# Kernel tuning notes

Hardware: AMD Instinct MI355X
Metric: run time of the kernel (lower is better)

The kernel has to match this reference:

```python
import jax, jax.numpy as jnp
import numpy as np

N, E = 50000, 800000
IN_FEATS, H, L = 16, 64, 3


def _glorot(key, shape):
    fan_in = shape[-1]
    return jax.random.normal(key, shape, dtype=jnp.float32) / np.sqrt(fan_in)


def setup_inputs() -> dict:
    key = jax.random.key(0)
    ks = jax.random.split(key, 12)
    return {
        "features": jax.random.normal(ks[0], (N, IN_FEATS), dtype=jnp.float32),
        "src": jax.random.randint(ks[1], (E,), 0, N, dtype=jnp.int32),
        "dst": jax.random.randint(ks[2], (E,), 0, N, dtype=jnp.int32),
        # input_module: Linear(in_feats, hidden)
        "W_in": _glorot(ks[3], (IN_FEATS, H)),
        "b_in": jnp.zeros((H,), jnp.float32),
        # edge_module: Linear(2*hidden, 1), shared across layers
        "W_edge": _glorot(ks[4], (2 * H, 1)),
        "b_edge": jnp.zeros((1,), jnp.float32),
        # per-layer GRUCell params (torch layout: [3H, H] for W_ih/W_hh)
        "Wih": _glorot(ks[5], (L, 3 * H, H)),
        "Whh": _glorot(ks[6], (L, 3 * H, H)),
        "bih": jnp.zeros((L, 3 * H), jnp.float32),
        "bhh": jnp.zeros((L, 3 * H), jnp.float32),
        # edge_predictor: Linear(2*hidden, 1)
        "W_pred": _glorot(ks[7], (2 * H, 1)),
        "b_pred": jnp.zeros((1,), jnp.float32),
    }


def _gru_cell(x, h, W_ih, W_hh, b_ih, b_hh):
    # torch.nn.GRUCell math
    gi = x @ W_ih.T + b_ih  # [N, 3H]
    gh = h @ W_hh.T + b_hh  # [N, 3H]
    i_r, i_z, i_n = jnp.split(gi, 3, axis=1)
    h_r, h_z, h_n = jnp.split(gh, 3, axis=1)
    r = jax.nn.sigmoid(i_r + h_r)
    z = jax.nn.sigmoid(i_z + h_z)
    n = jnp.tanh(i_n + r * h_n)
    return (1.0 - z) * n + z * h


def reference(features, src, dst, W_in, b_in, W_edge, b_edge, Wih, Whh, bih, bhh, W_pred, b_pred):
    n_nodes = features.shape[0]
    h = features @ W_in + b_in  # [N, H]
    num_layers = Wih.shape[0]
    for l in range(num_layers):
        h_u = h[src]  # [E, H] gather src
        h_v = h[dst]  # [E, H] gather dst
        # shared edge module: sigmoid(Linear(cat[h_u, h_v]))
        w = jax.nn.sigmoid(jnp.concatenate([h_u, h_v], axis=1) @ W_edge + b_edge)  # [E, 1]
        m = h_u * w  # messages [E, H]
        h_new = jax.ops.segment_sum(m, dst, num_segments=n_nodes)  # scatter-sum to dst
        h = _gru_cell(h_new, h, Wih[l], Whh[l], bih[l], bhh[l])
    edges_h = jnp.concatenate([h[src], h[dst]], axis=1)  # [E, 2H]
    return (edges_h @ W_pred + b_pred).squeeze()  # [E]
```

## Files before the change

### kernel.cpp

```cpp
#include <hip/hip_runtime.h>
#include <hip/hip_bf16.h>

#define H 64
#define H3 192
#define ITEMS 16

typedef __attribute__((ext_vector_type(8))) short short8;
typedef __attribute__((ext_vector_type(4))) float f32x4;

__device__ __forceinline__ float sigmoidf_(float x) {
    return 1.0f / (1.0f + __expf(-x));
}
__device__ __forceinline__ float tanhf_(float x) {
    float e = __expf(2.0f * x);
    return 1.0f - 2.0f / (e + 1.0f);
}
__device__ __forceinline__ unsigned short f2bf(float f) {
    unsigned u = __builtin_bit_cast(unsigned, f);
    u += 0x7FFFu + ((u >> 16) & 1u);
    return (unsigned short)(u >> 16);
}
__device__ __forceinline__ float bf2f(unsigned short s) {
    return __builtin_bit_cast(float, (unsigned)s << 16);
}

__global__ __launch_bounds__(256) void setup_kernel(
    const float* __restrict__ feat, const float* __restrict__ Win,
    const float* __restrict__ bin, const float* __restrict__ Wg,
    unsigned short* __restrict__ h_bf,
    float* __restrict__ a_gate, float* __restrict__ b_gate,
    const float* __restrict__ Wih, const float* __restrict__ Whh,
    unsigned short* __restrict__ w_bf,
    const int* __restrict__ dst, int* __restrict__ bhist,
    int N, int E, int per, int nbA, int nbB, int nb_c)
{
    int bid = blockIdx.x;
    int t = threadIdx.x;
    if (bid < nbA) {
        __shared__ float sWin[16 * H];
        __shared__ float sbin[H];
        __shared__ float sWg[2 * H];
        for (int i = t; i < 16 * H; i += 256) sWin[i] = Win[i];
        if (t < H) sbin[t] = bin[t];
        if (t < 2 * H) sWg[t] = Wg[t];
        __syncthreads();

        int n = bid * 256 + t;
        if (n >= N) return;

        float f[16];
        const float4* fr = (const float4*)(feat + (size_t)n * 16);
#pragma unroll
        for (int i = 0; i < 4; i++) {
            float4 v = fr[i];
            f[4 * i + 0] = v.x; f[4 * i + 1] = v.y;
            f[4 * i + 2] = v.z; f[4 * i + 3] = v.w;
        }
        float a = 0.f, b = 0.f;
        unsigned short* brow = h_bf + (size_t)n * H;
        for (int j = 0; j < H; j++) {
            float hj = sbin[j];
#pragma unroll
            for (int k = 0; k < 16; k++) hj += f[k] * sWin[k * H + j];
            brow[j] = f2bf(hj);
            a += hj * sWg[j];
            b += hj * sWg[H + j];
        }
        a_gate[n] = a;
        b_gate[n] = b;
    } else if (bid < nbA + nbB) {
        int i = (bid - nbA) * 256 + t;
        if (i < per) w_bf[i] = f2bf(Wih[i]);
        else if (i < 2 * per) w_bf[i] = f2bf(Whh[i - per]);
    } else {
        __shared__ int lh[256];
        lh[t] = 0;
        __syncthreads();
        int base = (bid - nbA - nbB) * (256 * ITEMS);
#pragma unroll
        for (int k = 0; k < ITEMS; k++) {
            int i = base + k * 256 + t;
            if (i < E) atomicAdd(&lh[dst[i] >> 8], 1);
        }
        __syncthreads();
        bhist[t * nb_c + (bid - nbA - nbB)] = lh[t];
    }
}

__global__ __launch_bounds__(256) void scan_fused(
    const int* __restrict__ bhist, int* __restrict__ S, int M, int E)
{
    int t = threadIdx.x;
    int b = blockIdx.x;
    int pre = b * 256;
    if (pre > M) pre = M;
    int v = 0;
    for (int k = t; k < pre; k += 256) v += bhist[k];
#pragma unroll
    for (int off = 32; off >= 1; off >>= 1) v += __shfl_xor(v, off);
    __shared__ int ws[4];
    if ((t & 63) == 0) ws[t >> 6] = v;
    __syncthreads();
    int carry = ws[0] + ws[1] + ws[2] + ws[3];

    int i = b * 256 + t;
    int x = (i < M) ? bhist[i] : 0;
    int lane = t & 63, w = t >> 6;
    int s = x;
#pragma unroll
    for (int off = 1; off < 64; off <<= 1) {
        int u = __shfl_up(s, off);
        if (lane >= off) s += u;
    }
    __shared__ int wsum[4];
    if (lane == 63) wsum[w] = s;
    __syncthreads();
    int add = 0;
    for (int k = 0; k < w; k++) add += wsum[k];
    if (i < M) S[i] = carry + s + add - x;
    else if (i == M) S[M] = E;
}

__global__ __launch_bounds__(256) void bucket_scatter_kernel(
    const int* __restrict__ src, const int* __restrict__ dst,
    const int* __restrict__ S, unsigned* __restrict__ pk, int E, int nb_c)
{
    __shared__ int lbase[256];
    __shared__ int lrun[256];
    int t = threadIdx.x;
    lbase[t] = S[t * nb_c + blockIdx.x];
    lrun[t] = 0;
    __syncthreads();
    int base = blockIdx.x * (256 * ITEMS);
#pragma unroll
    for (int k = 0; k < ITEMS; k++) {
        int i = base + k * 256 + t;
        if (i < E) {
            int d = dst[i];
            int b = d >> 8;
            int r = atomicAdd(&lrun[b], 1);
            pk[lbase[b] + r] = ((unsigned)(d & 255) << 16) | (unsigned)src[i];
        }
    }
}

__global__ __launch_bounds__(256) void bucket_finalize_kernel(
    const unsigned* __restrict__ pk, const int* __restrict__ S,
    int* __restrict__ offsets, unsigned short* __restrict__ csr16,
    int N, int E, int nb_c, int NB)
{
    __shared__ int lh[256];
    __shared__ int loff[256];
    __shared__ int lrun[256];
    int t = threadIdx.x;
    int b = blockIdx.x;
    int beg = S[b * nb_c];
    int endb = (b + 1 < NB) ? S[(b + 1) * nb_c] : E;
    lh[t] = 0; lrun[t] = 0;
    __syncthreads();
    for (int i = beg + t; i < endb; i += 256) atomicAdd(&lh[pk[i] >> 16], 1);
    __syncthreads();
    int v = lh[t];
    loff[t] = v;
    __syncthreads();
    for (int off = 1; off < 256; off <<= 1) {
        int u = (t >= off) ? loff[t - off] : 0;
        __syncthreads();
        loff[t] += u;
        __syncthreads();
    }
    int excl = loff[t] - v;
    int node = b * 256 + t;
    if (node < N) offsets[node] = beg + excl;
    if (b == NB - 1 && t == 0) offsets[N] = E;
    loff[t] = excl;
    __syncthreads();
    for (int i = beg + t; i < endb; i += 256) {
        unsigned w = pk[i];
        int d = (int)(w >> 16);
        int r = atomicAdd(&lrun[d], 1);
        csr16[beg + loff[d] + r] = (unsigned short)(w & 0xFFFFu);
    }
}

__global__ __launch_bounds__(256) void aggregate_kernel(
    const unsigned short* __restrict__ h_bf, const float* __restrict__ a_gate,
    const float* __restrict__ b_gate, const int* __restrict__ offsets,
    const unsigned short* __restrict__ csr16, const float* __restrict__ b_edge,
    unsigned short* __restrict__ hnew_bf, int N)
{
    int wid = threadIdx.x >> 6;
    int lane = threadIdx.x & 63;
    int sub = lane >> 3;
    int cg  = lane & 7;
    int v = blockIdx.x * 4 + wid;
    if (v >= N) return;

    int beg = offsets[v];
    int end = offsets[v + 1];
    float bv = b_gate[v] + b_edge[0];
    float acc0[8] = {0.f, 0.f, 0.f, 0.f, 0.f, 0.f, 0.f, 0.f};
    float acc1[8] = {0.f, 0.f, 0.f, 0.f, 0.f, 0.f, 0.f, 0.f};

    for (int cs = beg; cs < end; cs += 64) {
        int m = end - cs; if (m > 64) m = 64;
        int u = 0; float w = 0.f;
        if (lane < m) {
            u = (int)csr16[cs + lane];
            w = sigmoidf_(a_gate[u] + bv);
        }
        for (int j = 0; j < m; j += 16) {
            int e0 = j + sub, e1 = j + 8 + sub;
            int u0 = __shfl(u, e0 & 63);
            float w0 = __shfl(w, e0 & 63);
            int u1 = __shfl(u, e1 & 63);
            float w1 = __shfl(w, e1 & 63);
            if (e0 >= m) w0 = 0.f;
            if (e1 >= m) w1 = 0.f;
            short8 hv0 = *(const short8*)(h_bf + (size_t)u0 * H + cg * 8);
            short8 hv1 = *(const short8*)(h_bf + (size_t)u1 * H + cg * 8);
#pragma unroll
            for (int k = 0; k < 8; k++)
                acc0[k] += w0 * bf2f((unsigned short)hv0[k]);
#pragma unroll
            for (int k = 0; k < 8; k++)
                acc1[k] += w1 * bf2f((unsigned short)hv1[k]);
        }
    }
#pragma unroll
    for (int k = 0; k < 8; k++) acc0[k] += acc1[k];
#pragma unroll
    for (int mm = 8; mm < 64; mm <<= 1) {
#pragma unroll
        for (int k = 0; k < 8; k++)
            acc0[k] += __shfl_xor(acc0[k], mm);
    }
    if (sub == 0) {
        short8 o;
#pragma unroll
        for (int k = 0; k < 8; k++) o[k] = (short)f2bf(acc0[k]);
        *(short8*)(hnew_bf + (size_t)v * H + cg * 8) = o;
    }
}

__global__ __launch_bounds__(256) void gru_mfma_kernel(
    const unsigned short* __restrict__ x_bf,
    unsigned short* __restrict__ h_bf,
    const unsigned short* __restrict__ wih_bf,
    const unsigned short* __restrict__ whh_bf,
    const float* __restrict__ bih, const float* __restrict__ bhh,
    const float* __restrict__ Wg,
    float* __restrict__ a_gate, float* __restrict__ b_gate, int N)
{
    int lane = threadIdx.x & 63;
    int wv = threadIdx.x >> 6;
    int c = lane & 15;
    int g = lane >> 4;
    int nbase = blockIdx.x * 64 + wv * 16;
    if (nbase >= N) return;

    int nrow = nbase + c;
    int nclamp = nrow < N ? nrow : (N - 1);

    short8 ax[2], ah[2];
#pragma unroll
    for (int ch = 0; ch < 2; ch++) {
        ax[ch] = *(const short8*)(x_bf + (size_t)nclamp * H + ch * 32 + g * 8);
        ah[ch] = *(const short8*)(h_bf + (size_t)nclamp * H + ch * 32 + g * 8);
    }

    f32x4 gi[12], gh[12];
#pragma unroll
    for (int jb = 0; jb < 12; jb++) {
        gi[jb] = (f32x4){0.f, 0.f, 0.f, 0.f};
        gh[jb] = (f32x4){0.f, 0.f, 0.f, 0.f};
    }

#pragma unroll
    for (int jb = 0; jb < 12; jb++) {
        const unsigned short* wi = wih_bf + (size_t)(jb * 16 + c) * H + g * 8;
        const unsigned short* wh = whh_bf + (size_t)(jb * 16 + c) * H + g * 8;
        short8 wi0 = *(const short8*)(wi);
        short8 wi1 = *(const short8*)(wi + 32);
        short8 wh0 = *(const short8*)(wh);
        short8 wh1 = *(const short8*)(wh + 32);
        gi[jb] = __builtin_amdgcn_mfma_f32_16x16x32_bf16(ax[0], wi0, gi[jb], 0, 0, 0);
        gi[jb] = __builtin_amdgcn_mfma_f32_16x16x32_bf16(ax[1], wi1, gi[jb], 0, 0, 0);
        gh[jb] = __builtin_amdgcn_mfma_f32_16x16x32_bf16(ah[0], wh0, gh[jb], 0, 0, 0);
        gh[jb] = __builtin_amdgcn_mfma_f32_16x16x32_bf16(ah[1], wh1, gh[jb], 0, 0, 0);
    }

    float pa[4] = {0.f, 0.f, 0.f, 0.f};
    float pb[4] = {0.f, 0.f, 0.f, 0.f};
#pragma unroll
    for (int jb = 0; jb < 4; jb++) {
        int j = jb * 16 + c;
        float br = bih[j] + bhh[j];
        float bz = bih[H + j] + bhh[H + j];
        float bin_ = bih[2 * H + j];
        float bhn_ = bhh[2 * H + j];
        float wga = Wg[j], wgb = Wg[H + j];
#pragma unroll
        for (int q = 0; q < 4; q++) {
            int node = nbase + g * 4 + q;
            float r = sigmoidf_(gi[jb][q] + gh[jb][q] + br);
            float z = sigmoidf_(gi[jb + 4][q] + gh[jb + 4][q] + bz);
            float nn = tanhf_(gi[jb + 8][q] + bin_ + r * (gh[jb + 8][q] + bhn_));
            size_t idx = (size_t)node * H + j;
            float hp = bf2f(h_bf[idx]);
            float ho = (1.0f - z) * nn + z * hp;
            h_bf[idx] = f2bf(ho);
            pa[q] += ho * wga;
            pb[q] += ho * wgb;
        }
    }
#pragma unroll
    for (int m = 1; m < 16; m <<= 1) {
#pragma unroll
        for (int q = 0; q < 4; q++) {
            pa[q] += __shfl_xor(pa[q], m);
            pb[q] += __shfl_xor(pb[q], m);
        }
    }
    if (c == 0) {
#pragma unroll
        for (int q = 0; q < 4; q++) {
            int node = nbase + g * 4 + q;
            a_gate[node] = pa[q];
            b_gate[node] = pb[q];
        }
    }
}

__global__ __launch_bounds__(256) void predict_kernel(
    const int* __restrict__ src, const int* __restrict__ dst,
    const float* __restrict__ pa, const float* __restrict__ pb,
    const float* __restrict__ b_pred, float* __restrict__ out, int E)
{
    int e4 = (blockIdx.x * 256 + threadIdx.x) * 4;
    float bp = b_pred[0];
    if (e4 + 3 < E) {
        int4 s = *(const int4*)(src + e4);
        int4 d = *(const int4*)(dst + e4);
        float4 o;
        o.x = pa[s.x] + pb[d.x] + bp;
        o.y = pa[s.y] + pb[d.y] + bp;
        o.z = pa[s.z] + pb[d.z] + bp;
        o.w = pa[s.w] + pb[d.w] + bp;
        *(float4*)(out + e4) = o;
    } else {
        for (int e = e4; e < E; e++)
            out[e] = pa[src[e]] + pb[dst[e]] + bp;
    }
}

extern "C" void kernel_launch(void* const* d_in, const int* in_sizes, int n_in,
                              void* d_out, int out_size, void* d_ws, size_t ws_size,
                              hipStream_t stream) {
    const float* features = (const float*)d_in[0];
    const int*   src      = (const int*)d_in[1];
    const int*   dst      = (const int*)d_in[2];
    const float* W_in     = (const float*)d_in[3];
    const float* b_in     = (const float*)d_in[4];
    const float* W_edge   = (const float*)d_in[5];
    const float* b_edge   = (const float*)d_in[6];
    const float* Wih      = (const float*)d_in[7];
    const float* Whh      = (const float*)d_in[8];
    const float* bih      = (const float*)d_in[9];
    const float* bhh      = (const float*)d_in[10];
    const float* W_pred   = (const float*)d_in[11];
    const float* b_pred   = (const float*)d_in[12];
    float* out = (float*)d_out;

    int N = in_sizes[0] / 16;
    int E = in_sizes[1];
    int L = in_sizes[7] / (H3 * H);
    int per = L * H3 * H;

    int nb_nodes = (N + 255) / 256;
    int nb_agg   = (N + 3) / 4;
    int nb_gru   = (N + 63) / 64;
    int nb_conv  = (2 * per + 255) / 256;
    int nb_pred  = (E + 1023) / 1024;

    int nb_c = (E + 256 * ITEMS - 1) / (256 * ITEMS);
    int NB   = (N + 255) / 256;
    int M    = 256 * nb_c;
    int nb_scan = (M + 1 + 255) / 256;

    unsigned short* h_bf = (unsigned short*)d_ws;
    unsigned short* hnew_bf = h_bf + (size_t)N * H;
    unsigned short* w_bf = hnew_bf + (size_t)N * H;
    float* a_gate = (float*)(w_bf + 2 * per);
    float* b_gate = a_gate + N;
    int* offsets  = (int*)(b_gate + N);
    unsigned* pk  = (unsigned*)(offsets + N + 1);
    unsigned short* csr16 = (unsigned short*)(pk + E);
    int* bhist = (int*)(csr16 + E);
    int* sbh   = bhist + M;

    setup_kernel<<<nb_nodes + nb_conv + nb_c, 256, 0, stream>>>(
        features, W_in, b_in, W_edge, h_bf, a_gate, b_gate,
        Wih, Whh, w_bf, dst, bhist,
        N, E, per, nb_nodes, nb_conv, nb_c);

    scan_fused<<<nb_scan, 256, 0, stream>>>(bhist, sbh, M, E);
    bucket_scatter_kernel<<<nb_c, 256, 0, stream>>>(src, dst, sbh, pk, E, nb_c);
    bucket_finalize_kernel<<<NB, 256, 0, stream>>>(pk, sbh, offsets, csr16, N, E, nb_c, NB);

    for (int l = 0; l < L; l++) {
        aggregate_kernel<<<nb_agg, 256, 0, stream>>>(
            h_bf, a_gate, b_gate, offsets, csr16, b_edge, hnew_bf, N);
        const float* Wg = (l < L - 1) ? W_edge : W_pred;
        gru_mfma_kernel<<<nb_gru, 256, 0, stream>>>(
            hnew_bf, h_bf,
            w_bf + (size_t)l * H3 * H,
            w_bf + (size_t)per + (size_t)l * H3 * H,
            bih + (size_t)l * H3, bhh + (size_t)l * H3,
            Wg, a_gate, b_gate, N);
    }

    predict_kernel<<<nb_pred, 256, 0, stream>>>(src, dst, a_gate, b_gate, b_pred, out, E);
}
```

Before: 256.1 us.

## Fuse aggregation and GRU into one per-layer kernel with ping-pong buffers

Merges the per-layer aggregate and GRU kernels into a single kernel. Each block aggregates 16 nodes into shared memory, then one wavefront runs the MFMA GRU on that tile. h and the gate arrays are now double-buffered so a layer reads the old state and writes the new one without racing. This removes one launch per layer and the global round trip of the aggregated features. The cost is that three of four wavefronts sit idle during the GRU phase, and every block reloads the GRU weights for only 16 nodes.

New measurement: 263.2 us. 1.03x slower.

```diff
diff --git a/kernel.cpp b/kernel.cpp
--- a/kernel.cpp
+++ b/kernel.cpp
@@ -183,80 +183,85 @@
     }
 }
 
-__global__ __launch_bounds__(256) void aggregate_kernel(
-    const unsigned short* __restrict__ h_bf, const float* __restrict__ a_gate,
-    const float* __restrict__ b_gate, const int* __restrict__ offsets,
-    const unsigned short* __restrict__ csr16, const float* __restrict__ b_edge,
-    unsigned short* __restrict__ hnew_bf, int N)
-{
-    int wid = threadIdx.x >> 6;
-    int lane = threadIdx.x & 63;
-    int sub = lane >> 3;
-    int cg  = lane & 7;
-    int v = blockIdx.x * 4 + wid;
-    if (v >= N) return;
-
-    int beg = offsets[v];
-    int end = offsets[v + 1];
-    float bv = b_gate[v] + b_edge[0];
-    float acc0[8] = {0.f, 0.f, 0.f, 0.f, 0.f, 0.f, 0.f, 0.f};
-    float acc1[8] = {0.f, 0.f, 0.f, 0.f, 0.f, 0.f, 0.f, 0.f};
-
-    for (int cs = beg; cs < end; cs += 64) {
-        int m = end - cs; if (m > 64) m = 64;
-        int u = 0; float w = 0.f;
-        if (lane < m) {
-            u = (int)csr16[cs + lane];
-            w = sigmoidf_(a_gate[u] + bv);
-        }
-        for (int j = 0; j < m; j += 16) {
-            int e0 = j + sub, e1 = j + 8 + sub;
-            int u0 = __shfl(u, e0 & 63);
-            float w0 = __shfl(w, e0 & 63);
-            int u1 = __shfl(u, e1 & 63);
-            float w1 = __shfl(w, e1 & 63);
-            if (e0 >= m) w0 = 0.f;
-            if (e1 >= m) w1 = 0.f;
-            short8 hv0 = *(const short8*)(h_bf + (size_t)u0 * H + cg * 8);
-            short8 hv1 = *(const short8*)(h_bf + (size_t)u1 * H + cg * 8);
-#pragma unroll
-            for (int k = 0; k < 8; k++)
-                acc0[k] += w0 * bf2f((unsigned short)hv0[k]);
-#pragma unroll
-            for (int k = 0; k < 8; k++)
-                acc1[k] += w1 * bf2f((unsigned short)hv1[k]);
-        }
-    }
-#pragma unroll
-    for (int k = 0; k < 8; k++) acc0[k] += acc1[k];
-#pragma unroll
-    for (int mm = 8; mm < 64; mm <<= 1) {
-#pragma unroll
-        for (int k = 0; k < 8; k++)
-            acc0[k] += __shfl_xor(acc0[k], mm);
-    }
-    if (sub == 0) {
-        short8 o;
-#pragma unroll
-        for (int k = 0; k < 8; k++) o[k] = (short)f2bf(acc0[k]);
-        *(short8*)(hnew_bf + (size_t)v * H + cg * 8) = o;
-    }
-}
-
-__global__ __launch_bounds__(256) void gru_mfma_kernel(
-    const unsigned short* __restrict__ x_bf,
-    unsigned short* __restrict__ h_bf,
+__global__ __launch_bounds__(256) void layer_kernel(
+    const unsigned short* __restrict__ h_in,
+    unsigned short* __restrict__ h_out,
+    const float* __restrict__ a_in, const float* __restrict__ b_in,
+    float* __restrict__ a_out, float* __restrict__ b_out,
+    const int* __restrict__ offsets, const unsigned short* __restrict__ csr16,
+    const float* __restrict__ b_edge,
     const unsigned short* __restrict__ wih_bf,
     const unsigned short* __restrict__ whh_bf,
     const float* __restrict__ bih, const float* __restrict__ bhh,
-    const float* __restrict__ Wg,
-    float* __restrict__ a_gate, float* __restrict__ b_gate, int N)
-{
-    int lane = threadIdx.x & 63;
-    int wv = threadIdx.x >> 6;
+    const float* __restrict__ Wg, int N)
+{
+    __shared__ unsigned short sx[16 * H];
+
+    int t = threadIdx.x;
+    int wv = t >> 6;
+    int lane = t & 63;
+    int sub = lane >> 3;
+    int cg  = lane & 7;
+    int nbase = blockIdx.x * 16;
+    float be = b_edge[0];
+
+    for (int r = 0; r < 4; r++) {
+        int lv = wv * 4 + r;
+        int v = nbase + lv;
+        if (v >= N) break;
+
+        int beg = offsets[v];
+        int end = offsets[v + 1];
+        float bv = b_in[v] + be;
+        float acc0[8] = {0.f, 0.f, 0.f, 0.f, 0.f, 0.f, 0.f, 0.f};
+        float acc1[8] = {0.f, 0.f, 0.f, 0.f, 0.f, 0.f, 0.f, 0.f};
+
+        for (int cs = beg; cs < end; cs += 64) {
+            int m = end - cs; if (m > 64) m = 64;
+            int u = 0; float w = 0.f;
+            if (lane < m) {
+                u = (int)csr16[cs + lane];
+                w = sigmoidf_(a_in[u] + bv);
+            }
+            for (int j = 0; j < m; j += 16) {
+                int e0 = j + sub, e1 = j + 8 + sub;
+                int u0 = __shfl(u, e0 & 63);
+                float w0 = __shfl(w, e0 & 63);
+                int u1 = __shfl(u, e1 & 63);
+                float w1 = __shfl(w, e1 & 63);
+                if (e0 >= m) w0 = 0.f;
+                if (e1 >= m) w1 = 0.f;
+                short8 hv0 = *(const short8*)(h_in + (size_t)u0 * H + cg * 8);
+                short8 hv1 = *(const short8*)(h_in + (size_t)u1 * H + cg * 8);
+#pragma unroll
+                for (int k = 0; k < 8; k++)
+                    acc0[k] += w0 * bf2f((unsigned short)hv0[k]);
+#pragma unroll
+                for (int k = 0; k < 8; k++)
+                    acc1[k] += w1 * bf2f((unsigned short)hv1[k]);
+            }
+        }
+#pragma unroll
+        for (int k = 0; k < 8; k++) acc0[k] += acc1[k];
+#pragma unroll
+        for (int mm = 8; mm < 64; mm <<= 1) {
+#pragma unroll
+            for (int k = 0; k < 8; k++)
+                acc0[k] += __shfl_xor(acc0[k], mm);
+        }
+        if (sub == 0) {
+            short8 o;
+#pragma unroll
+            for (int k = 0; k < 8; k++) o[k] = (short)f2bf(acc0[k]);
+            *(short8*)(&sx[lv * H + cg * 8]) = o;
+        }
+    }
+    __syncthreads();
+
+    if (wv != 0) return;
+
     int c = lane & 15;
     int g = lane >> 4;
-    int nbase = blockIdx.x * 64 + wv * 16;
     if (nbase >= N) return;
 
     int nrow = nbase + c;
@@ -265,8 +270,8 @@
     short8 ax[2], ah[2];
 #pragma unroll
     for (int ch = 0; ch < 2; ch++) {
-        ax[ch] = *(const short8*)(x_bf + (size_t)nclamp * H + ch * 32 + g * 8);
-        ah[ch] = *(const short8*)(h_bf + (size_t)nclamp * H + ch * 32 + g * 8);
+        ax[ch] = *(const short8*)(&sx[c * H + ch * 32 + g * 8]);
+        ah[ch] = *(const short8*)(h_in + (size_t)nclamp * H + ch * 32 + g * 8);
     }
 
     f32x4 gi[12], gh[12];
@@ -303,13 +308,14 @@
 #pragma unroll
         for (int q = 0; q < 4; q++) {
             int node = nbase + g * 4 + q;
+            if (node >= N) continue;
             float r = sigmoidf_(gi[jb][q] + gh[jb][q] + br);
             float z = sigmoidf_(gi[jb + 4][q] + gh[jb + 4][q] + bz);
             float nn = tanhf_(gi[jb + 8][q] + bin_ + r * (gh[jb + 8][q] + bhn_));
             size_t idx = (size_t)node * H + j;
-            float hp = bf2f(h_bf[idx]);
+            float hp = bf2f(h_in[idx]);
             float ho = (1.0f - z) * nn + z * hp;
-            h_bf[idx] = f2bf(ho);
+            h_out[idx] = f2bf(ho);
             pa[q] += ho * wga;
             pb[q] += ho * wgb;
         }
@@ -326,8 +332,10 @@
 #pragma unroll
         for (int q = 0; q < 4; q++) {
             int node = nbase + g * 4 + q;
-            a_gate[node] = pa[q];
-            b_gate[node] = pb[q];
+            if (node < N) {
+                a_out[node] = pa[q];
+                b_out[node] = pb[q];
+            }
         }
     }
 }
@@ -378,29 +386,30 @@
     int per = L * H3 * H;
 
     int nb_nodes = (N + 255) / 256;
-    int nb_agg   = (N + 3) / 4;
-    int nb_gru   = (N + 63) / 64;
     int nb_conv  = (2 * per + 255) / 256;
     int nb_pred  = (E + 1023) / 1024;
+    int nb_layer = (N + 15) / 16;
 
     int nb_c = (E + 256 * ITEMS - 1) / (256 * ITEMS);
     int NB   = (N + 255) / 256;
     int M    = 256 * nb_c;
     int nb_scan = (M + 1 + 255) / 256;
 
-    unsigned short* h_bf = (unsigned short*)d_ws;
-    unsigned short* hnew_bf = h_bf + (size_t)N * H;
-    unsigned short* w_bf = hnew_bf + (size_t)N * H;
-    float* a_gate = (float*)(w_bf + 2 * per);
-    float* b_gate = a_gate + N;
-    int* offsets  = (int*)(b_gate + N);
+    unsigned short* hA = (unsigned short*)d_ws;
+    unsigned short* hB = hA + (size_t)N * H;
+    unsigned short* w_bf = hB + (size_t)N * H;
+    float* aA = (float*)(w_bf + 2 * per);
+    float* bA = aA + N;
+    float* aB = bA + N;
+    float* bB = aB + N;
+    int* offsets  = (int*)(bB + N);
     unsigned* pk  = (unsigned*)(offsets + N + 1);
     unsigned short* csr16 = (unsigned short*)(pk + E);
     int* bhist = (int*)(csr16 + E);
     int* sbh   = bhist + M;
 
     setup_kernel<<<nb_nodes + nb_conv + nb_c, 256, 0, stream>>>(
-        features, W_in, b_in, W_edge, h_bf, a_gate, b_gate,
+        features, W_in, b_in, W_edge, hA, aA, bA,
         Wih, Whh, w_bf, dst, bhist,
         N, E, per, nb_nodes, nb_conv, nb_c);
 
@@ -408,17 +417,22 @@
     bucket_scatter_kernel<<<nb_c, 256, 0, stream>>>(src, dst, sbh, pk, E, nb_c);
     bucket_finalize_kernel<<<NB, 256, 0, stream>>>(pk, sbh, offsets, csr16, N, E, nb_c, NB);
 
+    unsigned short* h_in = hA;  unsigned short* h_out = hB;
+    float *a_in = aA, *b_in2 = bA, *a_out = aB, *b_out = bB;
     for (int l = 0; l < L; l++) {
-        aggregate_kernel<<<nb_agg, 256, 0, stream>>>(
-            h_bf, a_gate, b_gate, offsets, csr16, b_edge, hnew_bf, N);
         const float* Wg = (l < L - 1) ? W_edge : W_pred;
-        gru_mfma_kernel<<<nb_gru, 256, 0, stream>>>(
-            hnew_bf, h_bf,
+        layer_kernel<<<nb_layer, 256, 0, stream>>>(
+            h_in, h_out, a_in, b_in2, a_out, b_out,
+            offsets, csr16, b_edge,
             w_bf + (size_t)l * H3 * H,
             w_bf + (size_t)per + (size_t)l * H3 * H,
             bih + (size_t)l * H3, bhh + (size_t)l * H3,
-            Wg, a_gate, b_gate, N);
-    }
-
-    predict_kernel<<<nb_pred, 256, 0, stream>>>(src, dst, a_gate, b_gate, b_pred, out, E);
-}
+            Wg, N);
+        unsigned short* th = h_in; h_in = h_out; h_out = th;
+        float* tf;
+        tf = a_in; a_in = a_out; a_out = tf;
+        tf = b_in2; b_in2 = b_out; b_out = tf;
+    }
+
+    predict_kernel<<<nb_pred, 256, 0, stream>>>(src, dst, a_in, b_in2, b_pred, out, E);
+}
```
